# Kernel optimization log

Measured on AMD Instinct MI355X. Metric: run time of the kernel, lower is better.

The kernel has to match this reference:

```python
import jax, jax.numpy as jnp
import numpy as np

N, K, C, SP = 65536, 16, 64, 8
C8 = C // SP  # attn_nn output dim == C // share_planes == 8
E = N * K
EPS = 1e-5


def _bn(x, g, b):
    # BatchNorm1d in training mode: batch statistics over the row dim
    mu = x.mean(0)
    var = ((x - mu) ** 2).mean(0)
    return (x - mu) * jax.lax.rsqrt(var + EPS) * g + b


def _segment_softmax(a, seg, n):
    m = jax.ops.segment_max(a, seg, num_segments=n)
    e = jnp.exp(a - m[seg])
    s = jax.ops.segment_sum(e, seg, num_segments=n)
    return e / s[seg]


def setup_inputs() -> dict:
    key = jax.random.key(0)
    ks = jax.random.split(key, 12)

    def w(k, shape, fan_in):
        return jax.random.normal(k, shape, jnp.float32) / np.sqrt(fan_in).astype(np.float32)

    x = jax.random.normal(ks[0], (N, C), jnp.float32)
    pos = jax.random.uniform(ks[1], (N, 3), jnp.float32)
    src = jax.random.randint(ks[2], (E,), 0, N)          # knn neighbor ids
    dst = jnp.repeat(jnp.arange(N), K)                   # k neighbors per target node
    edge_index = jnp.stack([src, dst]).astype(jnp.int32)
    return dict(
        x=x, pos=pos, edge_index=edge_index,
        W_in=w(ks[3], (C, C), C), W_out=w(ks[4], (C, C), C),
        pos_w1=w(ks[5], (3, 3), 3), pos_b1=jnp.zeros(3, jnp.float32),
        pos_bn_g=jnp.ones(3, jnp.float32), pos_bn_b=jnp.zeros(3, jnp.float32),
        pos_w2=w(ks[6], (C, 3), 3), pos_b2=jnp.zeros(C, jnp.float32),
        attn_bn1_g=jnp.ones(C, jnp.float32), attn_bn1_b=jnp.zeros(C, jnp.float32),
        attn_w1=w(ks[7], (C8, C), C), attn_b1=jnp.zeros(C8, jnp.float32),
        attn_bn2_g=jnp.ones(C8, jnp.float32), attn_bn2_b=jnp.zeros(C8, jnp.float32),
        attn_w2=w(ks[8], (C8, C8), C8), attn_b2=jnp.zeros(C8, jnp.float32),
        lin_w=w(ks[9], (C, C), C), lin_b=jnp.zeros(C, jnp.float32),
        src_w=w(ks[10], (C, C), C), src_b=jnp.zeros(C, jnp.float32),
        dst_w=w(ks[11], (C, C), C), dst_b=jnp.zeros(C, jnp.float32),
        bn1_g=jnp.ones(C, jnp.float32), bn1_b=jnp.zeros(C, jnp.float32),
        bn2_g=jnp.ones(C, jnp.float32), bn2_b=jnp.zeros(C, jnp.float32),
        bn3_g=jnp.ones(C, jnp.float32), bn3_b=jnp.zeros(C, jnp.float32),
    )


def reference(x, pos, edge_index, W_in, W_out, pos_w1, pos_b1, pos_bn_g, pos_bn_b,
              pos_w2, pos_b2, attn_bn1_g, attn_bn1_b, attn_w1, attn_b1,
              attn_bn2_g, attn_bn2_b, attn_w2, attn_b2, lin_w, lin_b,
              src_w, src_b, dst_w, dst_b, bn1_g, bn1_b, bn2_g, bn2_b, bn3_g, bn3_b):
    src, dst = edge_index[0], edge_index[1]
    x_skip = x
    # lin_in + bn1 + relu
    h = jax.nn.relu(_bn(x @ W_in.T, bn1_g, bn1_b))

    # --- PointTransformerConv ---
    a_src = h @ src_w.T + src_b
    a_dst = h @ dst_w.T + dst_b
    hW = h @ lin_w.T + lin_b

    rel = pos[src] - pos[dst]              # pos_j - pos_i  [E,3]
    d = jax.nn.relu(_bn(rel @ pos_w1.T + pos_b1, pos_bn_g, pos_bn_b))
    delta = d @ pos_w2.T + pos_b2          # [E,C]

    a = a_src[src] - a_dst[dst] + delta    # alpha_j - alpha_i + delta  [E,C]
    # attn_nn: BN -> ReLU -> (Lin C->C8, BN, ReLU) -> Lin C8->C8
    a = jax.nn.relu(_bn(a, attn_bn1_g, attn_bn1_b))
    a = jax.nn.relu(_bn(a @ attn_w1.T + attn_b1, attn_bn2_g, attn_bn2_b))
    a = a @ attn_w2.T + attn_b2            # [E,C8]
    alpha = _segment_softmax(a, dst, N)    # softmax over each node's neighborhood

    # grouped weighting with share_planes: [E,SP,C8] * [E,1,C8]
    msg = (alpha[:, None, :] * (hW[src] + delta).reshape(E, SP, C8)).reshape(E, C)
    out = jax.ops.segment_sum(msg, dst, num_segments=N)  # aggr='add'

    h2 = jax.nn.relu(_bn(out, bn2_g, bn2_b))
    h3 = _bn(h2 @ W_out.T, bn3_g, bn3_b)
    return jax.nn.relu(h3 + x_skip)
```

## Files before the change

kernel.cpp:

```cpp
#include <hip/hip_runtime.h>
#include <cstddef>

constexpr int N_ = 65536;
constexpr int K_ = 16;
constexpr int E_ = N_ * K_;
constexpr int C_ = 64;
#define EPS_ 1e-5f
#define SW 68
#define INV_N (1.f / 65536.f)
#define INV_E (1.f / 1048576.f)
#define NSLOT 64

typedef unsigned int uint_t;
typedef float f32x4_t __attribute__((ext_vector_type(4)));
typedef short bf16x8_t __attribute__((ext_vector_type(8)));

__device__ __forceinline__ uint_t bf16_rne(float f) {
    uint_t u = __float_as_uint(f);
    return (u + 0x7fffu + ((u >> 16) & 1u)) >> 16;
}
__device__ __forceinline__ float bf16_lo(uint_t p) { return __uint_as_float(p << 16); }
__device__ __forceinline__ float bf16_hi(uint_t p) { return __uint_as_float(p & 0xffff0000u); }
__device__ __forceinline__ uint_t pk2(float a, float b) {
    return bf16_rne(a) | (bf16_rne(b) << 16);
}

__device__ __forceinline__ void bn_ss(const float* __restrict__ s, int nchp, int c,
                                      float invM, const float* __restrict__ g,
                                      const float* __restrict__ b,
                                      float& sc, float& sh)
{
    float mean = s[c] * invM;
    float var  = fmaxf(s[nchp + c] * invM - mean * mean, 0.f);
    sc = g[c] * rsqrtf(var + EPS_);
    sh = b[c] - mean * sc;
}

__global__ void k_zero(float* __restrict__ p, int n)
{
    int i = blockIdx.x * 1024 + threadIdx.x;
    if (i < n) p[i] = 0.f;
}

__device__ __forceinline__ void stage_x(const float* __restrict__ in,
                                        const float* __restrict__ ss,
                                        float* __restrict__ Xs, int row0, int t)
{
#pragma unroll
    for (int it = 0; it < 4; ++it) {
        int m = t + 256 * it;
        int r = m >> 4, j = m & 15;
        float4 v = ((const float4*)in)[(size_t)(row0 + r) * 16 + j];
        if (ss) {
            float4 sc = ((const float4*)ss)[j];
            float4 sh = ((const float4*)(ss + 64))[j];
            v.x = fmaxf(fmaf(v.x, sc.x, sh.x), 0.f);
            v.y = fmaxf(fmaf(v.y, sc.y, sh.y), 0.f);
            v.z = fmaxf(fmaf(v.z, sc.z, sh.z), 0.f);
            v.w = fmaxf(fmaf(v.w, sc.w, sh.w), 0.f);
        }
        *(float4*)&Xs[r * SW + 4 * j] = v;
    }
}

__device__ __forceinline__ void stage_w(const float* __restrict__ W,
                                        float* __restrict__ Ws, int t)
{
#pragma unroll
    for (int it = 0; it < 4; ++it) {
        int m = t + 256 * it;
        int r = m >> 4, j = m & 15;
        *(float4*)&Ws[r * SW + 4 * j] = ((const float4*)W)[m];
    }
}

__device__ __forceinline__ void compute_tile(const float* __restrict__ Xs,
                                             const float* __restrict__ Ws,
                                             int tx, int ty, float acc[4][4])
{
#pragma unroll
    for (int r = 0; r < 4; ++r)
#pragma unroll
        for (int c = 0; c < 4; ++c) acc[r][c] = 0.f;
    for (int kc = 0; kc < 16; ++kc) {
        float4 xf[4], wf[4];
#pragma unroll
        for (int r = 0; r < 4; ++r)
            xf[r] = *(const float4*)&Xs[(tx + 16 * r) * SW + 4 * kc];
#pragma unroll
        for (int c = 0; c < 4; ++c)
            wf[c] = *(const float4*)&Ws[(ty + 16 * c) * SW + 4 * kc];
#pragma unroll
        for (int r = 0; r < 4; ++r)
#pragma unroll
            for (int c = 0; c < 4; ++c) {
                acc[r][c] = fmaf(xf[r].x, wf[c].x, acc[r][c]);
                acc[r][c] = fmaf(xf[r].y, wf[c].y, acc[r][c]);
                acc[r][c] = fmaf(xf[r].z, wf[c].z, acc[r][c]);
                acc[r][c] = fmaf(xf[r].w, wf[c].w, acc[r][c]);
            }
    }
}

__device__ __forceinline__ void write_tile(float* __restrict__ buf, int tx, int ty,
                                           const float acc[4][4],
                                           const float* __restrict__ bias,
                                           float* __restrict__ out, int row0, int t)
{
    __syncthreads();
#pragma unroll
    for (int r = 0; r < 4; ++r)
#pragma unroll
        for (int c = 0; c < 4; ++c)
            buf[(tx + 16 * r) * SW + ty + 16 * c] = acc[r][c];
    __syncthreads();
#pragma unroll
    for (int it = 0; it < 4; ++it) {
        int m = t + 256 * it;
        int r = m >> 4, j = m & 15;
        float4 v = *(const float4*)&buf[r * SW + 4 * j];
        if (bias) {
            float4 bv = ((const float4*)bias)[j];
            v.x += bv.x; v.y += bv.y; v.z += bv.z; v.w += bv.w;
        }
        ((float4*)out)[(size_t)(row0 + r) * 16 + j] = v;
    }
    __syncthreads();
}

__device__ __forceinline__ void write_tile_bf16(float* __restrict__ buf, int tx, int ty,
                                                const float acc[4][4],
                                                const float* __restrict__ bias,
                                                unsigned short* __restrict__ out,
                                                int row0, int t)
{
    __syncthreads();
#pragma unroll
    for (int r = 0; r < 4; ++r)
#pragma unroll
        for (int c = 0; c < 4; ++c)
            buf[(tx + 16 * r) * SW + ty + 16 * c] = acc[r][c];
    __syncthreads();
#pragma unroll
    for (int it = 0; it < 4; ++it) {
        int m = t + 256 * it;
        int r = m >> 4, j = m & 15;
        float4 v = *(const float4*)&buf[r * SW + 4 * j];
        if (bias) {
            float4 bv = ((const float4*)bias)[j];
            v.x += bv.x; v.y += bv.y; v.z += bv.z; v.w += bv.w;
        }
        uint2 o;
        o.x = bf16_rne(v.x) | (bf16_rne(v.y) << 16);
        o.y = bf16_rne(v.z) | (bf16_rne(v.w) << 16);
        ((uint2*)out)[(size_t)(row0 + r) * 16 + j] = o;
    }
    __syncthreads();
}

__global__ __launch_bounds__(256)
void k_gemm_tile(const float* __restrict__ in, const float* __restrict__ W,
                 const float* __restrict__ acc_in, const float* __restrict__ g_in,
                 const float* __restrict__ b_in, float invM_in,
                 float* __restrict__ out, float* __restrict__ acc_out)
{
    __shared__ float Xs[64 * SW];
    __shared__ float Ws[64 * SW];
    __shared__ float ssm[128];
    __shared__ float raws[128];
    int t = threadIdx.x, tx = t & 15, ty = t >> 4;
    int row0 = blockIdx.x * 64;
    if (acc_in) {
        if (t < 128) {
            float s = 0.f;
            for (int sl = 0; sl < NSLOT; ++sl) s += acc_in[sl * 128 + t];
            raws[t] = s;
        }
        __syncthreads();
        if (t < 64) {
            float scv, shv;
            bn_ss(raws, 64, t, invM_in, g_in, b_in, scv, shv);
            ssm[t] = scv; ssm[64 + t] = shv;
        }
    }
    __syncthreads();
    stage_x(in, acc_in ? ssm : nullptr, Xs, row0, t);
    stage_w(W, Ws, t);
    __syncthreads();
    float acc[4][4];
    compute_tile(Xs, Ws, tx, ty, acc);
    __syncthreads();
#pragma unroll
    for (int r = 0; r < 4; ++r)
#pragma unroll
        for (int c = 0; c < 4; ++c)
            Ws[(tx + 16 * r) * SW + ty + 16 * c] = acc[r][c];
    __syncthreads();
    float s0 = 0, s1 = 0, s2 = 0, s3 = 0, q0 = 0, q1 = 0, q2 = 0, q3 = 0;
#pragma unroll
    for (int it = 0; it < 4; ++it) {
        int m = t + 256 * it;
        int r = m >> 4, j = m & 15;
        float4 v = *(const float4*)&Ws[r * SW + 4 * j];
        ((float4*)out)[(size_t)(row0 + r) * 16 + j] = v;
        s0 += v.x; q0 = fmaf(v.x, v.x, q0);
        s1 += v.y; q1 = fmaf(v.y, v.y, q1);
        s2 += v.z; q2 = fmaf(v.z, v.z, q2);
        s3 += v.w; q3 = fmaf(v.w, v.w, q3);
    }
    float4* scr = (float4*)Xs;
    scr[t]       = make_float4(s0, s1, s2, s3);
    scr[256 + t] = make_float4(q0, q1, q2, q3);
    __syncthreads();
    if (t < 16) {
        float4 S = make_float4(0, 0, 0, 0), Q = make_float4(0, 0, 0, 0);
#pragma unroll
        for (int k = 0; k < 16; ++k) {
            float4 a = scr[k * 16 + t], b = scr[256 + k * 16 + t];
            S.x += a.x; S.y += a.y; S.z += a.z; S.w += a.w;
            Q.x += b.x; Q.y += b.y; Q.z += b.z; Q.w += b.w;
        }
        float* ao = acc_out + (blockIdx.x & (NSLOT - 1)) * 128;
        atomicAdd(&ao[4 * t + 0], S.x); atomicAdd(&ao[4 * t + 1], S.y);
        atomicAdd(&ao[4 * t + 2], S.z); atomicAdd(&ao[4 * t + 3], S.w);
        atomicAdd(&ao[64 + 4 * t + 0], Q.x); atomicAdd(&ao[64 + 4 * t + 1], Q.y);
        atomicAdd(&ao[64 + 4 * t + 2], Q.z); atomicAdd(&ao[64 + 4 * t + 3], Q.w);
    }
}

__global__ __launch_bounds__(256)
void k_gemm3_tile(const float* __restrict__ y, const float* __restrict__ acc1,
                  const float* __restrict__ g1, const float* __restrict__ b1,
                  const float* __restrict__ Wa, const float* __restrict__ ba,
                  const float* __restrict__ Wb, const float* __restrict__ bb,
                  const float* __restrict__ Wc, const float* __restrict__ bc,
                  unsigned short* __restrict__ oa16, float* __restrict__ ob,
                  unsigned short* __restrict__ oc16)
{
    __shared__ float Xs[64 * SW];
    __shared__ float Ws[64 * SW];
    __shared__ float ssm[128];
    __shared__ float raws[128];
    int t = threadIdx.x, tx = t & 15, ty = t >> 4;
    int row0 = blockIdx.x * 64;
    if (t < 128) {
        float s = 0.f;
        for (int sl = 0; sl < NSLOT; ++sl) s += acc1[sl * 128 + t];
        raws[t] = s;
    }
    __syncthreads();
    if (t < 64) {
        float scv, shv;
        bn_ss(raws, 64, t, INV_N, g1, b1, scv, shv);
        ssm[t] = scv; ssm[64 + t] = shv;
    }
    __syncthreads();
    stage_x(y, ssm, Xs, row0, t);
    stage_w(Wa, Ws, t);
    __syncthreads();
    float acc[4][4];
    compute_tile(Xs, Ws, tx, ty, acc);
    write_tile_bf16(Ws, tx, ty, acc, ba, oa16, row0, t);
    stage_w(Wb, Ws, t);
    __syncthreads();
    compute_tile(Xs, Ws, tx, ty, acc);
    write_tile(Ws, tx, ty, acc, bb, ob, row0, t);
    stage_w(Wc, Ws, t);
    __syncthreads();
    compute_tile(Xs, Ws, tx, ty, acc);
    write_tile_bf16(Ws, tx, ty, acc, bc, oc16, row0, t);
}

__global__ __launch_bounds__(256)
void k_pos_stats(const float* __restrict__ pos, const int* __restrict__ src,
                 const float* __restrict__ pw1, const float* __restrict__ pb1,
                 float* __restrict__ acc)
{
    float s0 = 0, s1 = 0, s2 = 0, q0 = 0, q1 = 0, q2 = 0;
    int tid = blockIdx.x * 256 + threadIdx.x;
    for (int e = tid; e < E_; e += 1024 * 256) {
        int si = src[e], di = e >> 4;
        float rx = pos[3 * si + 0] - pos[3 * di + 0];
        float ry = pos[3 * si + 1] - pos[3 * di + 1];
        float rz = pos[3 * si + 2] - pos[3 * di + 2];
        float u0 = fmaf(rx, pw1[0], fmaf(ry, pw1[1], fmaf(rz, pw1[2], pb1[0])));
        float u1 = fmaf(rx, pw1[3], fmaf(ry, pw1[4], fmaf(rz, pw1[5], pb1[1])));
        float u2 = fmaf(rx, pw1[6], fmaf(ry, pw1[7], fmaf(rz, pw1[8], pb1[2])));
        s0 += u0; q0 = fmaf(u0, u0, q0);
        s1 += u1; q1 = fmaf(u1, u1, q1);
        s2 += u2; q2 = fmaf(u2, u2, q2);
    }
#pragma unroll
    for (int m = 1; m < 64; m <<= 1) {
        s0 += __shfl_xor(s0, m, 64); s1 += __shfl_xor(s1, m, 64); s2 += __shfl_xor(s2, m, 64);
        q0 += __shfl_xor(q0, m, 64); q1 += __shfl_xor(q1, m, 64); q2 += __shfl_xor(q2, m, 64);
    }
    __shared__ float red[4][8];
    int wv = threadIdx.x >> 6, ln = threadIdx.x & 63;
    if (ln == 0) {
        red[wv][0] = s0; red[wv][1] = s1; red[wv][2] = s2; red[wv][3] = 0.f;
        red[wv][4] = q0; red[wv][5] = q1; red[wv][6] = q2; red[wv][7] = 0.f;
    }
    __syncthreads();
    if (threadIdx.x < 8)
        atomicAdd(&acc[(blockIdx.x & (NSLOT - 1)) * 32 + threadIdx.x],
                  red[0][threadIdx.x] + red[1][threadIdx.x] + red[2][threadIdx.x] + red[3][threadIdx.x]);
}

__global__ __launch_bounds__(256)
void k_abn1_stats(const float* __restrict__ pos, const int* __restrict__ src,
                  const unsigned short* __restrict__ asrc16,
                  const float* __restrict__ adst,
                  const float* __restrict__ pw1, const float* __restrict__ pb1,
                  const float* __restrict__ accpos, const float* __restrict__ pbg,
                  const float* __restrict__ pbb, const float* __restrict__ pw2,
                  const float* __restrict__ pb2, float* __restrict__ acc_a1)
{
    __shared__ float rawP[8];
    int t = threadIdx.x;
    int l = t & 15, g = t >> 4, wv = t >> 6;
    int c0 = 4 * l;
    if (t < 8) {
        float s = 0.f;
        for (int sl = 0; sl < NSLOT; ++sl) s += accpos[sl * 32 + t];
        rawP[t] = s;
    }
    __syncthreads();
    float ps0, ph0, ps1, ph1, ps2, ph2;
    bn_ss(rawP, 4, 0, INV_E, pbg, pbb, ps0, ph0);
    bn_ss(rawP, 4, 1, INV_E, pbg, pbb, ps1, ph1);
    bn_ss(rawP, 4, 2, INV_E, pbg, pbb, ps2, ph2);
    float4 p0 = *(const float4*)(pw2 + 12 * l);
    float4 p1 = *(const float4*)(pw2 + 12 * l + 4);
    float4 p2 = *(const float4*)(pw2 + 12 * l + 8);
    float4 pb = *(const float4*)(pb2 + c0);
    float sa0 = 0, sa1 = 0, sa2 = 0, sa3 = 0;
    float qa0 = 0, qa1 = 0, qa2 = 0, qa3 = 0;
#pragma unroll
    for (int nn = 0; nn < 2; ++nn) {
        int n = blockIdx.x * 32 + nn * 16 + g;
        float4 dv = *(const float4*)(adst + (size_t)n * 64 + c0);
        float pnx = pos[3 * n + 0], pny = pos[3 * n + 1], pnz = pos[3 * n + 2];
        int si_l = src[n * 16 + l];
        float rx = pos[3 * si_l + 0] - pnx;
        float ry = pos[3 * si_l + 1] - pny;
        float rz = pos[3 * si_l + 2] - pnz;
        float u0 = fmaf(rx, pw1[0], fmaf(ry, pw1[1], fmaf(rz, pw1[2], pb1[0])));
        float u1 = fmaf(rx, pw1[3], fmaf(ry, pw1[4], fmaf(rz, pw1[5], pb1[1])));
        float u2 = fmaf(rx, pw1[6], fmaf(ry, pw1[7], fmaf(rz, pw1[8], pb1[2])));
        float dl0 = fmaxf(fmaf(u0, ps0, ph0), 0.f);
        float dl1 = fmaxf(fmaf(u1, ps1, ph1), 0.f);
        float dl2 = fmaxf(fmaf(u2, ps2, ph2), 0.f);
        for (int k = 0; k < 16; ++k) {
            int si = __shfl(si_l, k, 16);
            float d0 = __shfl(dl0, k, 16);
            float d1 = __shfl(dl1, k, 16);
            float d2 = __shfl(dl2, k, 16);
            uint2 raw = ((const uint2*)asrc16)[(size_t)si * 16 + l];
            float avx = bf16_lo(raw.x), avy = bf16_hi(raw.x);
            float avz = bf16_lo(raw.y), avw = bf16_hi(raw.y);
            float del0 = fmaf(d0, p0.x, fmaf(d1, p0.y, fmaf(d2, p0.z, pb.x)));
            float del1 = fmaf(d0, p0.w, fmaf(d1, p1.x, fmaf(d2, p1.y, pb.y)));
            float del2 = fmaf(d0, p1.z, fmaf(d1, p1.w, fmaf(d2, p2.x, pb.z)));
            float del3 = fmaf(d0, p2.y, fmaf(d1, p2.z, fmaf(d2, p2.w, pb.w)));
            float a0 = avx - dv.x + del0;
            float a1 = avy - dv.y + del1;
            float a2 = avz - dv.z + del2;
            float a3 = avw - dv.w + del3;
            sa0 += a0; qa0 = fmaf(a0, a0, qa0);
            sa1 += a1; qa1 = fmaf(a1, a1, qa1);
            sa2 += a2; qa2 = fmaf(a2, a2, qa2);
            sa3 += a3; qa3 = fmaf(a3, a3, qa3);
        }
    }
#pragma unroll
    for (int m = 16; m <= 32; m <<= 1) {
        sa0 += __shfl_xor(sa0, m, 64); sa1 += __shfl_xor(sa1, m, 64);
        sa2 += __shfl_xor(sa2, m, 64); sa3 += __shfl_xor(sa3, m, 64);
        qa0 += __shfl_xor(qa0, m, 64); qa1 += __shfl_xor(qa1, m, 64);
        qa2 += __shfl_xor(qa2, m, 64); qa3 += __shfl_xor(qa3, m, 64);
    }
    __shared__ float red[4][128];
    if ((t & 63) < 16) {
        red[wv][c0 + 0] = sa0; red[wv][c0 + 1] = sa1;
        red[wv][c0 + 2] = sa2; red[wv][c0 + 3] = sa3;
        red[wv][64 + c0 + 0] = qa0; red[wv][64 + c0 + 1] = qa1;
        red[wv][64 + c0 + 2] = qa2; red[wv][64 + c0 + 3] = qa3;
    }
    __syncthreads();
    if (t < 128)
        atomicAdd(&acc_a1[(blockIdx.x & (NSLOT - 1)) * 128 + t],
                  red[0][t] + red[1][t] + red[2][t] + red[3][t]);
}

__global__ __launch_bounds__(256)
void k_edge_t1(const float* __restrict__ pos, const int* __restrict__ src,
               const unsigned short* __restrict__ asrc16,
               const float* __restrict__ adst,
               const float* __restrict__ pw1, const float* __restrict__ pb1,
               const float* __restrict__ accpos, const float* __restrict__ pbg,
               const float* __restrict__ pbb, const float* __restrict__ pw2,
               const float* __restrict__ pb2, const float* __restrict__ acc_a1,
               const float* __restrict__ a1g, const float* __restrict__ a1b,
               const float* __restrict__ aw1, const float* __restrict__ ab1,
               float* __restrict__ t1, float* __restrict__ acc_a2)
{
    __shared__ uint2 an_lds[4096];
    __shared__ float rawA1[128];
    __shared__ float rawP[8];
    __shared__ float red[4][16];
    int t = threadIdx.x;
    int l = t & 15, g = t >> 4, wv = t >> 6;
    int L = t & 63;
    int c0 = 4 * l;
    if (t < 128) {
        float s = 0.f;
        for (int sl = 0; sl < NSLOT; ++sl) s += acc_a1[sl * 128 + t];
        rawA1[t] = s;
    } else if (t < 136) {
        int i = t - 128;
        float s = 0.f;
        for (int sl = 0; sl < NSLOT; ++sl) s += accpos[sl * 32 + i];
        rawP[i] = s;
    }
    __syncthreads();
    float ps0, ph0, ps1, ph1, ps2, ph2;
    bn_ss(rawP, 4, 0, INV_E, pbg, pbb, ps0, ph0);
    bn_ss(rawP, 4, 1, INV_E, pbg, pbb, ps1, ph1);
    bn_ss(rawP, 4, 2, INV_E, pbg, pbb, ps2, ph2);
    float scx, shx, scy, shy, scz, shz, scw, shw;
    bn_ss(rawA1, 64, c0 + 0, INV_E, a1g, a1b, scx, shx);
    bn_ss(rawA1, 64, c0 + 1, INV_E, a1g, a1b, scy, shy);
    bn_ss(rawA1, 64, c0 + 2, INV_E, a1g, a1b, scz, shz);
    bn_ss(rawA1, 64, c0 + 3, INV_E, a1g, a1b, scw, shw);
    float4 p0 = *(const float4*)(pw2 + 12 * l);
    float4 p1 = *(const float4*)(pw2 + 12 * l + 4);
    float4 p2 = *(const float4*)(pw2 + 12 * l + 8);
    float4 pb = *(const float4*)(pb2 + c0);
    int col = L & 15, kb = L >> 4;
    uint4 bf0 = make_uint4(0u, 0u, 0u, 0u);
    uint4 bf1 = make_uint4(0u, 0u, 0u, 0u);
    float biasc = 0.f;
    if (col < 8) {
        const float* wr = aw1 + col * 64 + kb * 8;
        bf0 = make_uint4(pk2(wr[0], wr[1]), pk2(wr[2], wr[3]),
                         pk2(wr[4], wr[5]), pk2(wr[6], wr[7]));
        const float* wr2 = wr + 32;
        bf1 = make_uint4(pk2(wr2[0], wr2[1]), pk2(wr2[2], wr2[3]),
                         pk2(wr2[4], wr2[5]), pk2(wr2[6], wr2[7]));
        biasc = ab1[col];
    }
    int ar = col;
    int aoff0 = ar * 128 + ((kb * 16) ^ ((ar & 7) << 4));
    int aoff1 = ar * 128 + ((64 + kb * 16) ^ ((ar & 7) << 4));
    char* anb = (char*)an_lds;
    float se = 0.f, sq = 0.f;
#pragma unroll
    for (int nn = 0; nn < 2; ++nn) {
        int n = blockIdx.x * 32 + nn * 16 + g;
        float4 dv = *(const float4*)(adst + (size_t)n * 64 + c0);
        float pnx = pos[3 * n + 0], pny = pos[3 * n + 1], pnz = pos[3 * n + 2];
        int si_l = src[n * 16 + l];
        float rx = pos[3 * si_l + 0] - pnx;
        float ry = pos[3 * si_l + 1] - pny;
        float rz = pos[3 * si_l + 2] - pnz;
        float u0 = fmaf(rx, pw1[0], fmaf(ry, pw1[1], fmaf(rz, pw1[2], pb1[0])));
        float u1 = fmaf(rx, pw1[3], fmaf(ry, pw1[4], fmaf(rz, pw1[5], pb1[1])));
        float u2 = fmaf(rx, pw1[6], fmaf(ry, pw1[7], fmaf(rz, pw1[8], pb1[2])));
        float dl0 = fmaxf(fmaf(u0, ps0, ph0), 0.f);
        float dl1 = fmaxf(fmaf(u1, ps1, ph1), 0.f);
        float dl2 = fmaxf(fmaf(u2, ps2, ph2), 0.f);
#pragma unroll
        for (int k = 0; k < 16; ++k) {
            int si = __shfl(si_l, k, 16);
            float d0 = __shfl(dl0, k, 16);
            float d1 = __shfl(dl1, k, 16);
            float d2 = __shfl(dl2, k, 16);
            uint2 raw = ((const uint2*)asrc16)[(size_t)si * 16 + l];
            float avx = bf16_lo(raw.x), avy = bf16_hi(raw.x);
            float avz = bf16_lo(raw.y), avw = bf16_hi(raw.y);
            float del0 = fmaf(d0, p0.x, fmaf(d1, p0.y, fmaf(d2, p0.z, pb.x)));
            float del1 = fmaf(d0, p0.w, fmaf(d1, p1.x, fmaf(d2, p1.y, pb.y)));
            float del2 = fmaf(d0, p1.z, fmaf(d1, p1.w, fmaf(d2, p2.x, pb.z)));
            float del3 = fmaf(d0, p2.y, fmaf(d1, p2.z, fmaf(d2, p2.w, pb.w)));
            float an0 = fmaxf(fmaf(avx - dv.x + del0, scx, shx), 0.f);
            float an1 = fmaxf(fmaf(avy - dv.y + del1, scy, shy), 0.f);
            float an2 = fmaxf(fmaf(avz - dv.z + del2, scz, shz), 0.f);
            float an3 = fmaxf(fmaf(avw - dv.w + del3, scw, shw), 0.f);
            int woff = g * 2048 + k * 128 + ((8 * l) ^ ((k & 7) << 4));
            *(uint2*)(anb + woff) = make_uint2(pk2(an0, an1), pk2(an2, an3));
        }
#pragma unroll
        for (int tt = 0; tt < 4; ++tt) {
            int g2 = (wv << 2) + tt;
            int tb = g2 * 2048;
            uint4 a0 = *(const uint4*)(anb + tb + aoff0);
            uint4 a1v = *(const uint4*)(anb + tb + aoff1);
            f32x4_t acc = {0.f, 0.f, 0.f, 0.f};
            acc = __builtin_amdgcn_mfma_f32_16x16x32_bf16(
                      *(const bf16x8_t*)&a0, *(const bf16x8_t*)&bf0, acc, 0, 0, 0);
            acc = __builtin_amdgcn_mfma_f32_16x16x32_bf16(
                      *(const bf16x8_t*)&a1v, *(const bf16x8_t*)&bf1, acc, 0, 0, 0);
            if (col < 8) {
                int n2 = blockIdx.x * 32 + nn * 16 + g2;
                float* op = t1 + (size_t)(n2 * 16 + kb * 4) * 8 + col;
#pragma unroll
                for (int j = 0; j < 4; ++j) {
                    float v = acc[j] + biasc;
                    op[j * 8] = v;
                    se += v; sq = fmaf(v, v, sq);
                }
            }
        }
    }
    se += __shfl_xor(se, 16, 64); sq += __shfl_xor(sq, 16, 64);
    se += __shfl_xor(se, 32, 64); sq += __shfl_xor(sq, 32, 64);
    if (L < 8) { red[wv][col] = se; red[wv][8 + col] = sq; }
    __syncthreads();
    if (t < 16)
        atomicAdd(&acc_a2[(blockIdx.x & (NSLOT - 1)) * 32 + t],
                  red[0][t] + red[1][t] + red[2][t] + red[3][t]);
}

__global__ __launch_bounds__(256)
void k_node_aggr(const float* __restrict__ pos, const int* __restrict__ src,
                 const float* __restrict__ t1, const float* __restrict__ acc_a2,
                 const float* __restrict__ a2g, const float* __restrict__ a2b,
                 const float* __restrict__ aw2, const float* __restrict__ ab2,
                 const unsigned short* __restrict__ hw16,
                 const float* __restrict__ accpos, const float* __restrict__ pbg,
                 const float* __restrict__ pbb,
                 const float* __restrict__ pw1, const float* __restrict__ pb1,
                 const float* __restrict__ pw2, const float* __restrict__ pb2,
                 float* __restrict__ out, float* __restrict__ acc_bn2)
{
    __shared__ float alds[16][196];
    __shared__ float ssm2[16];
    __shared__ float rawA2[16];
    __shared__ float rawP[8];
    int t = threadIdx.x, l = t & 15, g = t >> 4;
    int c0 = 4 * l;
    if (t < 16) {
        float s = 0.f;
        for (int sl = 0; sl < NSLOT; ++sl) s += acc_a2[sl * 32 + t];
        rawA2[t] = s;
    } else if (t < 24) {
        int i = t - 16;
        float s = 0.f;
        for (int sl = 0; sl < NSLOT; ++sl) s += accpos[sl * 32 + i];
        rawP[i] = s;
    }
    __syncthreads();
    if (t < 8) {
        float scv, shv;
        bn_ss(rawA2, 8, t, INV_E, a2g, a2b, scv, shv);
        ssm2[t] = scv; ssm2[8 + t] = shv;
    }
    __syncthreads();
    float ps0, ph0, ps1, ph1, ps2, ph2;
    bn_ss(rawP, 4, 0, INV_E, pbg, pbb, ps0, ph0);
    bn_ss(rawP, 4, 1, INV_E, pbg, pbb, ps1, ph1);
    bn_ss(rawP, 4, 2, INV_E, pbg, pbb, ps2, ph2);
    float4 p0 = *(const float4*)(pw2 + 12 * l);
    float4 p1 = *(const float4*)(pw2 + 12 * l + 4);
    float4 p2 = *(const float4*)(pw2 + 12 * l + 8);
    float4 pb = *(const float4*)(pb2 + c0);
    int alof = (l & 1) * 4;
    int n = blockIdx.x * 16 + g;
    int e = n * 16 + l;
    const float4* t4 = (const float4*)(t1 + (size_t)e * 8);
    float4 ta = t4[0], tb = t4[1];
    float tv[8] = {ta.x, ta.y, ta.z, ta.w, tb.x, tb.y, tb.z, tb.w};
    float tn[8];
#pragma unroll
    for (int j = 0; j < 8; ++j)
        tn[j] = fmaxf(fmaf(tv[j], ssm2[j], ssm2[8 + j]), 0.f);
    float al[8];
#pragma unroll
    for (int j = 0; j < 8; ++j) {
        float acc = ab2[j];
#pragma unroll
        for (int i = 0; i < 8; ++i) acc = fmaf(tn[i], aw2[j * 8 + i], acc);
        float m = acc;
#pragma unroll
        for (int msk = 1; msk < 16; msk <<= 1) m = fmaxf(m, __shfl_xor(m, msk, 64));
        float ex = __expf(acc - m);
        float sm = ex;
#pragma unroll
        for (int msk = 1; msk < 16; msk <<= 1) sm += __shfl_xor(sm, msk, 64);
        al[j] = ex / sm;
    }
    *(float4*)&alds[g][l * 12]     = make_float4(al[0], al[1], al[2], al[3]);
    *(float4*)&alds[g][l * 12 + 4] = make_float4(al[4], al[5], al[6], al[7]);
    int silane = src[e];
    float pnx = pos[3 * n + 0], pny = pos[3 * n + 1], pnz = pos[3 * n + 2];
    float rx = pos[3 * silane + 0] - pnx;
    float ry = pos[3 * silane + 1] - pny;
    float rz = pos[3 * silane + 2] - pnz;
    float u0 = fmaf(rx, pw1[0], fmaf(ry, pw1[1], fmaf(rz, pw1[2], pb1[0])));
    float u1 = fmaf(rx, pw1[3], fmaf(ry, pw1[4], fmaf(rz, pw1[5], pb1[1])));
    float u2 = fmaf(rx, pw1[6], fmaf(ry, pw1[7], fmaf(rz, pw1[8], pb1[2])));
    float dl0 = fmaxf(fmaf(u0, ps0, ph0), 0.f);
    float dl1 = fmaxf(fmaf(u1, ps1, ph1), 0.f);
    float dl2 = fmaxf(fmaf(u2, ps2, ph2), 0.f);
    float a0 = 0.f, a1 = 0.f, a2 = 0.f, a3 = 0.f;
#pragma unroll 4
    for (int k = 0; k < 16; ++k) {
        int sk = __shfl(silane, k, 16);
        float d0 = __shfl(dl0, k, 16);
        float d1 = __shfl(dl1, k, 16);
        float d2 = __shfl(dl2, k, 16);
        uint2 raw = ((const uint2*)hw16)[(size_t)sk * 16 + l];
        float hvx = bf16_lo(raw.x), hvy = bf16_hi(raw.x);
        float hvz = bf16_lo(raw.y), hvw = bf16_hi(raw.y);
        float4 alv = *(const float4*)&alds[g][k * 12 + alof];
        float del0 = fmaf(d0, p0.x, fmaf(d1, p0.y, fmaf(d2, p0.z, pb.x)));
        float del1 = fmaf(d0, p0.w, fmaf(d1, p1.x, fmaf(d2, p1.y, pb.y)));
        float del2 = fmaf(d0, p1.z, fmaf(d1, p1.w, fmaf(d2, p2.x, pb.z)));
        float del3 = fmaf(d0, p2.y, fmaf(d1, p2.z, fmaf(d2, p2.w, pb.w)));
        a0 = fmaf(alv.x, hvx + del0, a0);
        a1 = fmaf(alv.y, hvy + del1, a1);
        a2 = fmaf(alv.z, hvz + del2, a2);
        a3 = fmaf(alv.w, hvw + del3, a3);
    }
    *(float4*)(out + (size_t)n * 64 + c0) = make_float4(a0, a1, a2, a3);
    __syncthreads();
    float4* scr = (float4*)&alds[0][0];
    scr[g * 16 + l]       = make_float4(a0, a1, a2, a3);
    scr[256 + g * 16 + l] = make_float4(a0 * a0, a1 * a1, a2 * a2, a3 * a3);
    __syncthreads();
    if (t < 16) {
        float4 S = make_float4(0, 0, 0, 0), Q = make_float4(0, 0, 0, 0);
#pragma unroll
        for (int k = 0; k < 16; ++k) {
            float4 a = scr[k * 16 + t], b = scr[256 + k * 16 + t];
            S.x += a.x; S.y += a.y; S.z += a.z; S.w += a.w;
            Q.x += b.x; Q.y += b.y; Q.z += b.z; Q.w += b.w;
        }
        float* ao = acc_bn2 + (blockIdx.x & (NSLOT - 1)) * 128;
        atomicAdd(&ao[4 * t + 0], S.x); atomicAdd(&ao[4 * t + 1], S.y);
        atomicAdd(&ao[4 * t + 2], S.z); atomicAdd(&ao[4 * t + 3], S.w);
        atomicAdd(&ao[64 + 4 * t + 0], Q.x); atomicAdd(&ao[64 + 4 * t + 1], Q.y);
        atomicAdd(&ao[64 + 4 * t + 2], Q.z); atomicAdd(&ao[64 + 4 * t + 3], Q.w);
    }
}

__global__ __launch_bounds__(256)
void k_final(const float* __restrict__ y3, const float* __restrict__ acc3,
             const float* __restrict__ g3, const float* __restrict__ b3,
             const float* __restrict__ x, float* __restrict__ out)
{
    __shared__ float raws[128];
    __shared__ float ssl[128];
    int t = threadIdx.x;
    if (t < 128) {
        float s = 0.f;
        for (int sl = 0; sl < NSLOT; ++sl) s += acc3[sl * 128 + t];
        raws[t] = s;
    }
    __syncthreads();
    if (t < 64) {
        float scv, shv;
        bn_ss(raws, 64, t, INV_N, g3, b3, scv, shv);
        ssl[t] = scv; ssl[64 + t] = shv;
    }
    __syncthreads();
    int i = blockIdx.x * 256 + t;
    int c4 = i & 15;
    float4 sc = *(const float4*)&ssl[4 * c4];
    float4 sh = *(const float4*)&ssl[64 + 4 * c4];
    float4 v  = ((const float4*)y3)[i];
    float4 xs = ((const float4*)x)[i];
    float4 o;
    o.x = fmaxf(fmaf(v.x, sc.x, sh.x) + xs.x, 0.f);
    o.y = fmaxf(fmaf(v.y, sc.y, sh.y) + xs.y, 0.f);
    o.z = fmaxf(fmaf(v.z, sc.z, sh.z) + xs.z, 0.f);
    o.w = fmaxf(fmaf(v.w, sc.w, sh.w) + xs.w, 0.f);
    ((float4*)out)[i] = o;
}

extern "C" void kernel_launch(void* const* d_in, const int* in_sizes, int n_in,
                              void* d_out, int out_size, void* d_ws, size_t ws_size,
                              hipStream_t stream)
{
    const float* x    = (const float*)d_in[0];
    const float* pos  = (const float*)d_in[1];
    const int*   src  = (const int*)d_in[2];
    const float* W_in = (const float*)d_in[3];
    const float* W_out= (const float*)d_in[4];
    const float* pw1  = (const float*)d_in[5];
    const float* pb1  = (const float*)d_in[6];
    const float* pbg  = (const float*)d_in[7];
    const float* pbb  = (const float*)d_in[8];
    const float* pw2  = (const float*)d_in[9];
    const float* pb2  = (const float*)d_in[10];
    const float* a1g  = (const float*)d_in[11];
    const float* a1b  = (const float*)d_in[12];
    const float* aw1  = (const float*)d_in[13];
    const float* ab1  = (const float*)d_in[14];
    const float* a2g  = (const float*)d_in[15];
    const float* a2b  = (const float*)d_in[16];
    const float* aw2  = (const float*)d_in[17];
    const float* ab2  = (const float*)d_in[18];
    const float* linw = (const float*)d_in[19];
    const float* linb = (const float*)d_in[20];
    const float* srcw = (const float*)d_in[21];
    const float* srcb = (const float*)d_in[22];
    const float* dstw = (const float*)d_in[23];
    const float* dstb = (const float*)d_in[24];
    const float* bn1g = (const float*)d_in[25];
    const float* bn1b = (const float*)d_in[26];
    const float* bn2g = (const float*)d_in[27];
    const float* bn2b = (const float*)d_in[28];
    const float* bn3g = (const float*)d_in[29];
    const float* bn3b = (const float*)d_in[30];
    float* outp = (float*)d_out;

    float* ws = (float*)d_ws;
    const size_t NC = (size_t)N_ * C_;
    float* buf_y     = ws;
    float* buf_adst  = ws + NC;
    unsigned short* asrc16 = (unsigned short*)(ws + 2 * NC);
    unsigned short* hw16   = (unsigned short*)(ws + 2 * NC + NC / 2);
    float* buf_t1    = ws + 3 * NC;
    float* accb      = ws + 3 * NC + (size_t)E_ * 8;
    float* acc_bn1 = accb;
    float* acc_pos = accb + 64 * 128;
    float* acc_a1  = acc_pos + 64 * 32;
    float* acc_a2  = acc_a1 + 64 * 128;
    float* acc_bn2 = acc_a2 + 64 * 32;
    float* acc_bn3 = acc_bn2 + 64 * 128;
    const int ACC_TOTAL = 64 * (128 + 32 + 128 + 32 + 128 + 128);
    float* buf_out = buf_adst;

    k_zero<<<(ACC_TOTAL + 1023) / 1024, 1024, 0, stream>>>(accb, ACC_TOTAL);
    k_gemm_tile<<<1024, 256, 0, stream>>>(x, W_in, nullptr, nullptr, nullptr, 0.f,
                                          buf_y, acc_bn1);
    k_gemm3_tile<<<1024, 256, 0, stream>>>(buf_y, acc_bn1, bn1g, bn1b,
                                           srcw, srcb, dstw, dstb, linw, linb,
                                           asrc16, buf_adst, hw16);
    k_pos_stats<<<1024, 256, 0, stream>>>(pos, src, pw1, pb1, acc_pos);
    k_abn1_stats<<<2048, 256, 0, stream>>>(pos, src, asrc16, buf_adst,
                                           pw1, pb1, acc_pos, pbg, pbb,
                                           pw2, pb2, acc_a1);
    k_edge_t1<<<2048, 256, 0, stream>>>(pos, src, asrc16, buf_adst,
                                        pw1, pb1, acc_pos, pbg, pbb, pw2, pb2,
                                        acc_a1, a1g, a1b, aw1, ab1,
                                        buf_t1, acc_a2);
    k_node_aggr<<<4096, 256, 0, stream>>>(pos, src, buf_t1, acc_a2, a2g, a2b,
                                          aw2, ab2, hw16, acc_pos, pbg, pbb,
                                          pw1, pb1, pw2, pb2, buf_out, acc_bn2);
    k_gemm_tile<<<1024, 256, 0, stream>>>(buf_out, W_out, acc_bn2, bn2g, bn2b, INV_N,
                                          buf_y, acc_bn3);
    k_final<<<(N_ * C_ / 4) / 256, 256, 0, stream>>>(buf_y, acc_bn3, bn3g, bn3b, x, outp);

    (void)in_sizes; (void)n_in; (void)out_size; (void)ws_size;
}
```

Before: 321.5 us.

## Build MFMA A-operand directly in registers, removing LDS staging in edge kernel

Restructures k_edge_t1 so each lane computes the eight bf16 activations that form its own MFMA A-fragment. The old path wrote to a swizzled LDS tile via shuffles and then read it back. BN scale is folded into the pos_w2 weights and into a combined bias, and a hardware packed bf16 convert replaces the software rounding. This drops the LDS round-trip and the per-edge shuffles. In exchange each lane does more gather loads per node with wider uint4 reads, and needs more registers for the folded weights.

```diff
diff --git a/kernel.cpp b/kernel.cpp
--- a/kernel.cpp
+++ b/kernel.cpp
@@ -23,6 +23,11 @@
 __device__ __forceinline__ float bf16_hi(uint_t p) { return __uint_as_float(p & 0xffff0000u); }
 __device__ __forceinline__ uint_t pk2(float a, float b) {
     return bf16_rne(a) | (bf16_rne(b) << 16);
+}
+__device__ __forceinline__ uint_t cvtpk(float lo, float hi) {
+    uint_t r;
+    asm("v_cvt_pk_bf16_f32 %0, %1, %2" : "=v"(r) : "v"(lo), "v"(hi));
+    return r;
 }
 
 __device__ __forceinline__ void bn_ss(const float* __restrict__ s, int nchp, int c,
@@ -405,14 +410,12 @@
                const float* __restrict__ aw1, const float* __restrict__ ab1,
                float* __restrict__ t1, float* __restrict__ acc_a2)
 {
-    __shared__ uint2 an_lds[4096];
     __shared__ float rawA1[128];
     __shared__ float rawP[8];
     __shared__ float red[4][16];
     int t = threadIdx.x;
-    int l = t & 15, g = t >> 4, wv = t >> 6;
-    int L = t & 63;
-    int c0 = 4 * l;
+    int wv = t >> 6, L = t & 63;
+    int col = L & 15, kb = L >> 4;
     if (t < 128) {
         float s = 0.f;
         for (int sl = 0; sl < NSLOT; ++sl) s += acc_a1[sl * 128 + t];
@@ -428,16 +431,30 @@
     bn_ss(rawP, 4, 0, INV_E, pbg, pbb, ps0, ph0);
     bn_ss(rawP, 4, 1, INV_E, pbg, pbb, ps1, ph1);
     bn_ss(rawP, 4, 2, INV_E, pbg, pbb, ps2, ph2);
-    float scx, shx, scy, shy, scz, shz, scw, shw;
-    bn_ss(rawA1, 64, c0 + 0, INV_E, a1g, a1b, scx, shx);
-    bn_ss(rawA1, 64, c0 + 1, INV_E, a1g, a1b, scy, shy);
-    bn_ss(rawA1, 64, c0 + 2, INV_E, a1g, a1b, scz, shz);
-    bn_ss(rawA1, 64, c0 + 3, INV_E, a1g, a1b, scw, shw);
-    float4 p0 = *(const float4*)(pw2 + 12 * l);
-    float4 p1 = *(const float4*)(pw2 + 12 * l + 4);
-    float4 p2 = *(const float4*)(pw2 + 12 * l + 8);
-    float4 pb = *(const float4*)(pb2 + c0);
-    int col = L & 15, kb = L >> 4;
+    float sc0[8], sc1[8], pbs0[8], pbs1[8];
+    {
+        float sh;
+#pragma unroll
+        for (int j = 0; j < 8; ++j) {
+            bn_ss(rawA1, 64, kb * 8 + j, INV_E, a1g, a1b, sc0[j], sh);
+            pbs0[j] = fmaf(pb2[kb * 8 + j], sc0[j], sh);
+            bn_ss(rawA1, 64, 32 + kb * 8 + j, INV_E, a1g, a1b, sc1[j], sh);
+            pbs1[j] = fmaf(pb2[32 + kb * 8 + j], sc1[j], sh);
+        }
+    }
+    float P0[24], P1[24];
+#pragma unroll
+    for (int q = 0; q < 6; ++q) {
+        float4 v = *(const float4*)(pw2 + 24 * kb + 4 * q);
+        P0[4*q+0] = v.x; P0[4*q+1] = v.y; P0[4*q+2] = v.z; P0[4*q+3] = v.w;
+        float4 w = *(const float4*)(pw2 + 96 + 24 * kb + 4 * q);
+        P1[4*q+0] = w.x; P1[4*q+1] = w.y; P1[4*q+2] = w.z; P1[4*q+3] = w.w;
+    }
+#pragma unroll
+    for (int j = 0; j < 8; ++j) {
+        P0[3*j+0] *= sc0[j]; P0[3*j+1] *= sc0[j]; P0[3*j+2] *= sc0[j];
+        P1[3*j+0] *= sc1[j]; P1[3*j+1] *= sc1[j]; P1[3*j+2] *= sc1[j];
+    }
     uint4 bf0 = make_uint4(0u, 0u, 0u, 0u);
     uint4 bf1 = make_uint4(0u, 0u, 0u, 0u);
     float biasc = 0.f;
@@ -450,66 +467,68 @@
                          pk2(wr2[4], wr2[5]), pk2(wr2[6], wr2[7]));
         biasc = ab1[col];
     }
-    int ar = col;
-    int aoff0 = ar * 128 + ((kb * 16) ^ ((ar & 7) << 4));
-    int aoff1 = ar * 128 + ((64 + kb * 16) ^ ((ar & 7) << 4));
-    char* anb = (char*)an_lds;
     float se = 0.f, sq = 0.f;
-#pragma unroll
-    for (int nn = 0; nn < 2; ++nn) {
-        int n = blockIdx.x * 32 + nn * 16 + g;
-        float4 dv = *(const float4*)(adst + (size_t)n * 64 + c0);
+    int n0 = blockIdx.x * 32 + wv * 8;
+#pragma unroll 2
+    for (int tt = 0; tt < 8; ++tt) {
+        int n = n0 + tt;
+        int si = src[n * 16 + col];
+        const char* ap = (const char*)asrc16 + (size_t)si * 128 + kb * 16;
+        uint4 ra = *(const uint4*)ap;
+        uint4 rb = *(const uint4*)(ap + 64);
+        const float* dp = adst + (size_t)n * 64 + kb * 8;
+        float4 dv00 = *(const float4*)dp;
+        float4 dv01 = *(const float4*)(dp + 4);
+        float4 dv10 = *(const float4*)(dp + 32);
+        float4 dv11 = *(const float4*)(dp + 36);
         float pnx = pos[3 * n + 0], pny = pos[3 * n + 1], pnz = pos[3 * n + 2];
-        int si_l = src[n * 16 + l];
-        float rx = pos[3 * si_l + 0] - pnx;
-        float ry = pos[3 * si_l + 1] - pny;
-        float rz = pos[3 * si_l + 2] - pnz;
+        float rx = pos[3 * si + 0] - pnx;
+        float ry = pos[3 * si + 1] - pny;
+        float rz = pos[3 * si + 2] - pnz;
         float u0 = fmaf(rx, pw1[0], fmaf(ry, pw1[1], fmaf(rz, pw1[2], pb1[0])));
         float u1 = fmaf(rx, pw1[3], fmaf(ry, pw1[4], fmaf(rz, pw1[5], pb1[1])));
         float u2 = fmaf(rx, pw1[6], fmaf(ry, pw1[7], fmaf(rz, pw1[8], pb1[2])));
-        float dl0 = fmaxf(fmaf(u0, ps0, ph0), 0.f);
-        float dl1 = fmaxf(fmaf(u1, ps1, ph1), 0.f);
-        float dl2 = fmaxf(fmaf(u2, ps2, ph2), 0.f);
-#pragma unroll
-        for (int k = 0; k < 16; ++k) {
-            int si = __shfl(si_l, k, 16);
-            float d0 = __shfl(dl0, k, 16);
-            float d1 = __shfl(dl1, k, 16);
-            float d2 = __shfl(dl2, k, 16);
-            uint2 raw = ((const uint2*)asrc16)[(size_t)si * 16 + l];
-            float avx = bf16_lo(raw.x), avy = bf16_hi(raw.x);
-            float avz = bf16_lo(raw.y), avw = bf16_hi(raw.y);
-            float del0 = fmaf(d0, p0.x, fmaf(d1, p0.y, fmaf(d2, p0.z, pb.x)));
-            float del1 = fmaf(d0, p0.w, fmaf(d1, p1.x, fmaf(d2, p1.y, pb.y)));
-            float del2 = fmaf(d0, p1.z, fmaf(d1, p1.w, fmaf(d2, p2.x, pb.z)));
-            float del3 = fmaf(d0, p2.y, fmaf(d1, p2.z, fmaf(d2, p2.w, pb.w)));
-            float an0 = fmaxf(fmaf(avx - dv.x + del0, scx, shx), 0.f);
-            float an1 = fmaxf(fmaf(avy - dv.y + del1, scy, shy), 0.f);
-            float an2 = fmaxf(fmaf(avz - dv.z + del2, scz, shz), 0.f);
-            float an3 = fmaxf(fmaf(avw - dv.w + del3, scw, shw), 0.f);
-            int woff = g * 2048 + k * 128 + ((8 * l) ^ ((k & 7) << 4));
-            *(uint2*)(anb + woff) = make_uint2(pk2(an0, an1), pk2(an2, an3));
-        }
-#pragma unroll
-        for (int tt = 0; tt < 4; ++tt) {
-            int g2 = (wv << 2) + tt;
-            int tb = g2 * 2048;
-            uint4 a0 = *(const uint4*)(anb + tb + aoff0);
-            uint4 a1v = *(const uint4*)(anb + tb + aoff1);
-            f32x4_t acc = {0.f, 0.f, 0.f, 0.f};
-            acc = __builtin_amdgcn_mfma_f32_16x16x32_bf16(
-                      *(const bf16x8_t*)&a0, *(const bf16x8_t*)&bf0, acc, 0, 0, 0);
-            acc = __builtin_amdgcn_mfma_f32_16x16x32_bf16(
-                      *(const bf16x8_t*)&a1v, *(const bf16x8_t*)&bf1, acc, 0, 0, 0);
-            if (col < 8) {
-                int n2 = blockIdx.x * 32 + nn * 16 + g2;
-                float* op = t1 + (size_t)(n2 * 16 + kb * 4) * 8 + col;
-#pragma unroll
-                for (int j = 0; j < 4; ++j) {
-                    float v = acc[j] + biasc;
-                    op[j * 8] = v;
-                    se += v; sq = fmaf(v, v, sq);
-                }
+        float d0 = fmaxf(fmaf(u0, ps0, ph0), 0.f);
+        float d1 = fmaxf(fmaf(u1, ps1, ph1), 0.f);
+        float d2 = fmaxf(fmaf(u2, ps2, ph2), 0.f);
+        float dvv0[8] = {dv00.x, dv00.y, dv00.z, dv00.w, dv01.x, dv01.y, dv01.z, dv01.w};
+        float dvv1[8] = {dv10.x, dv10.y, dv10.z, dv10.w, dv11.x, dv11.y, dv11.z, dv11.w};
+        float av0[8], av1[8];
+        av0[0] = bf16_lo(ra.x); av0[1] = bf16_hi(ra.x);
+        av0[2] = bf16_lo(ra.y); av0[3] = bf16_hi(ra.y);
+        av0[4] = bf16_lo(ra.z); av0[5] = bf16_hi(ra.z);
+        av0[6] = bf16_lo(ra.w); av0[7] = bf16_hi(ra.w);
+        av1[0] = bf16_lo(rb.x); av1[1] = bf16_hi(rb.x);
+        av1[2] = bf16_lo(rb.y); av1[3] = bf16_hi(rb.y);
+        av1[4] = bf16_lo(rb.z); av1[5] = bf16_hi(rb.z);
+        av1[6] = bf16_lo(rb.w); av1[7] = bf16_hi(rb.w);
+        float an0[8], an1[8];
+#pragma unroll
+        for (int j = 0; j < 8; ++j) {
+            float q0 = fmaf(-dvv0[j], sc0[j], pbs0[j]);
+            float de0 = fmaf(d0, P0[3*j], fmaf(d1, P0[3*j+1], fmaf(d2, P0[3*j+2], q0)));
+            an0[j] = fmaxf(fmaf(av0[j], sc0[j], de0), 0.f);
+            float q1 = fmaf(-dvv1[j], sc1[j], pbs1[j]);
+            float de1 = fmaf(d0, P1[3*j], fmaf(d1, P1[3*j+1], fmaf(d2, P1[3*j+2], q1)));
+            an1[j] = fmaxf(fmaf(av1[j], sc1[j], de1), 0.f);
+        }
+        uint4 af0, af1;
+        af0.x = cvtpk(an0[0], an0[1]); af0.y = cvtpk(an0[2], an0[3]);
+        af0.z = cvtpk(an0[4], an0[5]); af0.w = cvtpk(an0[6], an0[7]);
+        af1.x = cvtpk(an1[0], an1[1]); af1.y = cvtpk(an1[2], an1[3]);
+        af1.z = cvtpk(an1[4], an1[5]); af1.w = cvtpk(an1[6], an1[7]);
+        f32x4_t acc = {0.f, 0.f, 0.f, 0.f};
+        acc = __builtin_amdgcn_mfma_f32_16x16x32_bf16(
+                  *(const bf16x8_t*)&af0, *(const bf16x8_t*)&bf0, acc, 0, 0, 0);
+        acc = __builtin_amdgcn_mfma_f32_16x16x32_bf16(
+                  *(const bf16x8_t*)&af1, *(const bf16x8_t*)&bf1, acc, 0, 0, 0);
+        if (col < 8) {
+            float* op = t1 + (size_t)(n * 16 + kb * 4) * 8 + col;
+#pragma unroll
+            for (int j = 0; j < 4; ++j) {
+                float v = acc[j] + biasc;
+                op[j * 8] = v;
+                se += v; sq = fmaf(v, v, sq);
             }
         }
     }
```

Result: faster. 314.9 us (-2.1%).
